# Performance work log

Measured on AMD Instinct MI355X. Metric: run time of the kernel, lower is better.

The kernel has to match this reference:

```python
import jax, jax.numpy as jnp
import numpy as np

EMB = 1024
HEADS = 16
HEAD_DIM = EMB // HEADS


def setup_inputs() -> dict:
    key = jax.random.key(0)
    ks = jax.random.split(key, 5)
    x = jax.random.normal(ks[0], (2, 2048, EMB), dtype=jnp.float32)
    # per-head projection params, stacked over heads: [H, E, D]
    Wq = jax.random.normal(ks[1], (HEADS, EMB, HEAD_DIM), dtype=jnp.float32)
    Wk = jax.random.normal(ks[2], (HEADS, EMB, HEAD_DIM), dtype=jnp.float32)
    Wv = jax.random.normal(ks[3], (HEADS, EMB, HEAD_DIM), dtype=jnp.float32)
    # output projection (torch Linear weight [out, in], bias=False)
    Wo = jax.random.normal(ks[4], (EMB, EMB), dtype=jnp.float32) * (1.0 / np.sqrt(EMB))
    return {"x": x, "Wq": Wq, "Wk": Wk, "Wv": Wv, "Wo": Wo}


def reference(x, Wq, Wk, Wv, Wo):
    B, T, E = x.shape
    # per-head projections: [B, H, T, D]
    q = jnp.einsum('bte,hed->bhtd', x, Wq)
    k = jnp.einsum('bte,hed->bhtd', x, Wk)
    v = jnp.einsum('bte,hed->bhtd', x, Wv)
    scale = 1.0 / jnp.sqrt(jnp.asarray(HEAD_DIM, dtype=x.dtype))
    scores = jnp.einsum('bhtd,bhsd->bhts', q, k) * scale  # [B,H,T,T]
    s = jax.nn.softmax(scores, axis=-1)
    out = jnp.einsum('bhts,bhsd->bhtd', s, v)
    # concat heads along last dim in head order: [B, T, H*D]
    combined = jnp.transpose(out, (0, 2, 1, 3)).reshape(B, T, E)
    # residual + output projection (Linear bias=False: y = combined @ Wo.T)
    return x + combined @ Wo.T
```

## Files before the change

kernel.cpp:

```cpp
#include <hip/hip_runtime.h>

#define EMB   1024
#define HEADS 16
#define HDIM  64
#define BATCH 2
#define SEQ   2048
#define MROWS (BATCH*SEQ)
#define STR   40
#define QSCALE 0.1803368801111204f

typedef __attribute__((ext_vector_type(8))) short bf16x8;
typedef __attribute__((ext_vector_type(4))) float f32x4;
typedef unsigned short u16;

__device__ __forceinline__ u16 f2bf(float f) {
    unsigned u = __float_as_uint(f);
    u += 0x7fffu + ((u >> 16) & 1u);
    return (u16)(u >> 16);
}
__device__ __forceinline__ float bf2f(u16 h) {
    return __uint_as_float((unsigned)h << 16);
}
__device__ __forceinline__ float fast_exp2(float x) {
#if __has_builtin(__builtin_amdgcn_exp2f)
    return __builtin_amdgcn_exp2f(x);
#else
    return __expf(x * 0.6931471805599453f);
#endif
}
__device__ __forceinline__ unsigned pk_trunc(float lo, float hi) {
    return __builtin_amdgcn_perm(__float_as_uint(hi), __float_as_uint(lo),
                                 0x07060302u);
}

#define SWZ(r, ch) ((((r) << 6)) + ((((ch) ^ ((r) & 7))) << 3))

__global__ __launch_bounds__(256)
void prep1(const float* __restrict__ X, const float* __restrict__ Wq,
           const float* __restrict__ Wk, const float* __restrict__ Wv,
           u16* __restrict__ Xh, u16* __restrict__ Xl,
           u16* __restrict__ Qth, u16* __restrict__ Qtl,
           u16* __restrict__ Kth, u16* __restrict__ Ktl,
           u16* __restrict__ Vth)
{
    const int bx = blockIdx.x;
    if (bx < 2048) {
        int i = (bx * 256 + threadIdx.x) * 8;
#pragma unroll
        for (int half = 0; half < 2; ++half) {
            float4 v = *(const float4*)(X + i + half * 4);
            ushort4 hi, lo;
            hi.x = f2bf(v.x); lo.x = f2bf(v.x - bf2f(hi.x));
            hi.y = f2bf(v.y); lo.y = f2bf(v.y - bf2f(hi.y));
            hi.z = f2bf(v.z); lo.z = f2bf(v.z - bf2f(hi.z));
            hi.w = f2bf(v.w); lo.w = f2bf(v.w - bf2f(hi.w));
            *(ushort4*)(Xh + i + half * 4) = hi;
            *(ushort4*)(Xl + i + half * 4) = lo;
        }
    } else if (bx < 3072) {
        const int f = bx - 2048;
        const int z = f >> 9, y = (f >> 5) & 15, x = f & 31;
        const float* W  = z ? Wk  : Wq;
        u16* Oh         = z ? Kth : Qth;
        u16* Ol         = z ? Ktl : Qtl;
        const int d  = threadIdx.x & 63;
        const int e0 = (x * 4 + (threadIdx.x >> 6)) * 8;
        const float* src = W + ((size_t)y * EMB + e0) * HDIM + d;
        ushort4 h0, h1, l0, l1;
        float v; u16 hv;
        v = src[0 * 64]; hv = f2bf(v); h0.x = hv; l0.x = f2bf(v - bf2f(hv));
        v = src[1 * 64]; hv = f2bf(v); h0.y = hv; l0.y = f2bf(v - bf2f(hv));
        v = src[2 * 64]; hv = f2bf(v); h0.z = hv; l0.z = f2bf(v - bf2f(hv));
        v = src[3 * 64]; hv = f2bf(v); h0.w = hv; l0.w = f2bf(v - bf2f(hv));
        v = src[4 * 64]; hv = f2bf(v); h1.x = hv; l1.x = f2bf(v - bf2f(hv));
        v = src[5 * 64]; hv = f2bf(v); h1.y = hv; l1.y = f2bf(v - bf2f(hv));
        v = src[6 * 64]; hv = f2bf(v); h1.z = hv; l1.z = f2bf(v - bf2f(hv));
        v = src[7 * 64]; hv = f2bf(v); h1.w = hv; l1.w = f2bf(v - bf2f(hv));
        size_t obase = ((size_t)y * HDIM + d) * EMB + e0;
        *(ushort4*)(Oh + obase)     = h0;
        *(ushort4*)(Oh + obase + 4) = h1;
        *(ushort4*)(Ol + obase)     = l0;
        *(ushort4*)(Ol + obase + 4) = l1;
    } else {
        const int f = bx - 3072;
        const int y = f >> 5, x = f & 31;
        const int d  = threadIdx.x & 63;
        const int e0 = (x * 4 + (threadIdx.x >> 6)) * 8;
        const float* src = Wv + ((size_t)y * EMB + e0) * HDIM + d;
        ushort4 h0, h1;
        h0.x = f2bf(src[0 * 64]); h0.y = f2bf(src[1 * 64]);
        h0.z = f2bf(src[2 * 64]); h0.w = f2bf(src[3 * 64]);
        h1.x = f2bf(src[4 * 64]); h1.y = f2bf(src[5 * 64]);
        h1.z = f2bf(src[6 * 64]); h1.w = f2bf(src[7 * 64]);
        size_t obase = ((size_t)y * HDIM + d) * EMB + e0;
        *(ushort4*)(Vth + obase)     = h0;
        *(ushort4*)(Vth + obase + 4) = h1;
    }
}

__global__ __launch_bounds__(256, 2)
void qkv_fused(const u16* __restrict__ Xh, const u16* __restrict__ Xl,
               const u16* __restrict__ Wqh, const u16* __restrict__ Wql,
               const u16* __restrict__ Wkh, const u16* __restrict__ Wkl,
               const u16* __restrict__ Wvt,
               u16* __restrict__ Qh, u16* __restrict__ Ql,
               u16* __restrict__ Kh, u16* __restrict__ Kl,
               u16* __restrict__ Vt)
{
    const int z  = blockIdx.z;
    const bool isV = (z == 2);
    const int m0 = blockIdx.x * 128;
    const int n0 = blockIdx.y * 128;
    const int t    = threadIdx.x;
    const int wave = t >> 6, lane = t & 63;
    const int wm = wave & 1, wn = wave >> 1;
    const int l16 = lane & 15, quad = lane >> 4;

    __shared__ u16 Ahs[128][STR];
    __shared__ u16 Als[128][STR];
    __shared__ u16 Bhs[128][STR];
    __shared__ u16 Bls[128][STR];

    const u16* Bh_g = isV ? Wvt : (z ? Wkh : Wqh);
    const u16* Bl_g = z ? Wkl : Wql;

    const int ar0 = t >> 2, ak = (t & 3) * 8, ar1 = ar0 + 64;

    f32x4 acc[4][4];
#pragma unroll
    for (int i = 0; i < 4; ++i)
#pragma unroll
        for (int j = 0; j < 4; ++j) acc[i][j] = (f32x4){0.f, 0.f, 0.f, 0.f};

    bf16x8 cur[8], nxt[8], nx2[8];
#define QK_LOAD(dst, kk)                                                            \
    do {                                                                            \
        dst[0] = *(const bf16x8*)(Xh  + (size_t)(m0 + ar0) * EMB + (kk) + ak);      \
        dst[1] = *(const bf16x8*)(Xh  + (size_t)(m0 + ar1) * EMB + (kk) + ak);      \
        dst[4] = *(const bf16x8*)(Bh_g + (size_t)(n0 + ar0) * EMB + (kk) + ak);     \
        dst[5] = *(const bf16x8*)(Bh_g + (size_t)(n0 + ar1) * EMB + (kk) + ak);     \
        if (!isV) {                                                                 \
            dst[2] = *(const bf16x8*)(Xl  + (size_t)(m0 + ar0) * EMB + (kk) + ak);  \
            dst[3] = *(const bf16x8*)(Xl  + (size_t)(m0 + ar1) * EMB + (kk) + ak);  \
            dst[6] = *(const bf16x8*)(Bl_g + (size_t)(n0 + ar0) * EMB + (kk) + ak); \
            dst[7] = *(const bf16x8*)(Bl_g + (size_t)(n0 + ar1) * EMB + (kk) + ak); \
        }                                                                           \
    } while (0)

    QK_LOAD(cur, 0);
    QK_LOAD(nxt, 32);

    for (int k0 = 0; k0 < EMB; k0 += 32) {
        __syncthreads();
        *(bf16x8*)&Ahs[ar0][ak] = cur[0];  *(bf16x8*)&Ahs[ar1][ak] = cur[1];
        *(bf16x8*)&Bhs[ar0][ak] = cur[4];  *(bf16x8*)&Bhs[ar1][ak] = cur[5];
        if (!isV) {
            *(bf16x8*)&Als[ar0][ak] = cur[2];  *(bf16x8*)&Als[ar1][ak] = cur[3];
            *(bf16x8*)&Bls[ar0][ak] = cur[6];  *(bf16x8*)&Bls[ar1][ak] = cur[7];
        }
        __syncthreads();

        const int kn = (k0 + 64 < EMB) ? k0 + 64 : 0;
        QK_LOAD(nx2, kn);

        bf16x8 B4h[4], B4l[4];
#pragma unroll
        for (int j = 0; j < 4; ++j) {
            B4h[j] = *(const bf16x8*)&Bhs[wn * 64 + 16 * j + l16][quad * 8];
            if (!isV)
                B4l[j] = *(const bf16x8*)&Bls[wn * 64 + 16 * j + l16][quad * 8];
        }
#pragma unroll
        for (int i = 0; i < 4; ++i) {
            bf16x8 Ai_h = *(const bf16x8*)&Ahs[wm * 64 + 16 * i + l16][quad * 8];
            if (!isV) {
                bf16x8 Ai_l = *(const bf16x8*)&Als[wm * 64 + 16 * i + l16][quad * 8];
#pragma unroll
                for (int j = 0; j < 4; ++j) {
                    acc[i][j] = __builtin_amdgcn_mfma_f32_16x16x32_bf16(Ai_h, B4h[j], acc[i][j], 0, 0, 0);
                    acc[i][j] = __builtin_amdgcn_mfma_f32_16x16x32_bf16(Ai_h, B4l[j], acc[i][j], 0, 0, 0);
                    acc[i][j] = __builtin_amdgcn_mfma_f32_16x16x32_bf16(Ai_l, B4h[j], acc[i][j], 0, 0, 0);
                }
            } else {
#pragma unroll
                for (int j = 0; j < 4; ++j)
                    acc[i][j] = __builtin_amdgcn_mfma_f32_16x16x32_bf16(Ai_h, B4h[j], acc[i][j], 0, 0, 0);
            }
        }
#pragma unroll
        for (int q = 0; q < 8; ++q) { cur[q] = nxt[q]; nxt[q] = nx2[q]; }
    }
#undef QK_LOAD

    const int b = m0 >> 11;
    const int h = (n0 + wn * 64) >> 6;
    if (isV) {
#pragma unroll
        for (int i = 0; i < 4; ++i)
#pragma unroll
            for (int j = 0; j < 4; ++j) {
                int d  = 16 * j + l16;
                int tt = (m0 & (SEQ - 1)) + wm * 64 + 16 * i + quad * 4;
                ushort4 o;
                o.x = f2bf(acc[i][j][0]); o.y = f2bf(acc[i][j][1]);
                o.z = f2bf(acc[i][j][2]); o.w = f2bf(acc[i][j][3]);
                *(ushort4*)(Vt + ((size_t)(b * HEADS + h) * HDIM + d) * SEQ + tt) = o;
            }
    } else {
        u16* Oh = z ? Kh : Qh;
        u16* Ol = z ? Kl : Ql;
        const float esc = z ? 1.0f : QSCALE;
#pragma unroll
        for (int i = 0; i < 4; ++i)
#pragma unroll
            for (int r = 0; r < 4; ++r) {
                int tt = (m0 & (SEQ - 1)) + wm * 64 + 16 * i + quad * 4 + r;
                size_t rowbase = ((size_t)(b * HEADS + h) * SEQ + tt) * HDIM;
#pragma unroll
                for (int j = 0; j < 4; ++j) {
                    int d = 16 * j + l16;
                    float v = acc[i][j][r] * esc;
                    u16 hv = f2bf(v);
                    Oh[rowbase + d] = hv;
                    Ol[rowbase + d] = f2bf(v - bf2f(hv));
                }
            }
    }
}

__global__ __launch_bounds__(256, 2)
void attn_mfma(const u16* __restrict__ Qh, const u16* __restrict__ Ql,
               const u16* __restrict__ Kh, const u16* __restrict__ Kl,
               const u16* __restrict__ Vt, u16* __restrict__ Cb,
               const float* __restrict__ Wo, u16* __restrict__ Woh)
{
    if (blockIdx.y == BATCH * HEADS) {
        int base = (blockIdx.x * 256 + threadIdx.x) * 8;
#pragma unroll 4
        for (int it = 0; it < 32; ++it) {
#pragma unroll
            for (int half = 0; half < 2; ++half) {
                float4 v = *(const float4*)(Wo + base + half * 4);
                ushort4 o;
                o.x = f2bf(v.x); o.y = f2bf(v.y); o.z = f2bf(v.z); o.w = f2bf(v.w);
                *(ushort4*)(Woh + base + half * 4) = o;
            }
            base += 16 * 256 * 8;
        }
        return;
    }

    const int qt0  = blockIdx.x * 128;
    const int bh   = blockIdx.y;
    const int t    = threadIdx.x;
    const int wave = t >> 6;
    const int lane = t & 63;
    const int l16  = lane & 15;
    const int quad = lane >> 4;

    __shared__ u16 Ksh[4096];
    __shared__ u16 Ksl[4096];
    __shared__ u16 Vs [4096];
    __shared__ u16 Ps [8192];

    const size_t bh_off = (size_t)bh * SEQ * HDIM;
    const u16* Qhb = Qh + bh_off;
    const u16* Qlb = Ql + bh_off;
    const u16* Khb = Kh + bh_off;
    const u16* Klb = Kl + bh_off;
    const u16* Vtb = Vt + bh_off;

    bf16x8 aQh[2][2], aQl[2][2];
#pragma unroll
    for (int g = 0; g < 2; ++g) {
        const int qrow = qt0 + g * 64 + wave * 16 + l16;
        const u16* bH = Qhb + (size_t)qrow * HDIM + quad * 8;
        const u16* bL = Qlb + (size_t)qrow * HDIM + quad * 8;
        aQh[g][0] = *(const bf16x8*)(bH);
        aQh[g][1] = *(const bf16x8*)(bH + 32);
        aQl[g][0] = *(const bf16x8*)(bL);
        aQl[g][1] = *(const bf16x8*)(bL + 32);
    }

    f32x4 accO[2][4];
    float m_i[2] = {-1e30f, -1e30f}, l_i[2] = {0.f, 0.f};
#pragma unroll
    for (int g = 0; g < 2; ++g)
#pragma unroll
        for (int j = 0; j < 4; ++j) accO[g][j] = (f32x4){0.f, 0.f, 0.f, 0.f};

    const int sr0 = t >> 3, sch = t & 7, sr1 = sr0 + 32;
    const int gc  = sch * 8;
    const int so0 = SWZ(sr0, sch), so1 = SWZ(sr1, sch);

    bf16x8 cur[6], nxt[6];
#define KV_LOAD(dst, ss)                                                       \
    do {                                                                       \
        dst[0] = *(const bf16x8*)(Khb + (size_t)((ss) + sr0) * HDIM + gc);     \
        dst[1] = *(const bf16x8*)(Khb + (size_t)((ss) + sr1) * HDIM + gc);     \
        dst[2] = *(const bf16x8*)(Klb + (size_t)((ss) + sr0) * HDIM + gc);     \
        dst[3] = *(const bf16x8*)(Klb + (size_t)((ss) + sr1) * HDIM + gc);     \
        dst[4] = *(const bf16x8*)(Vtb + (size_t)sr0 * SEQ + (ss) + gc);        \
        dst[5] = *(const bf16x8*)(Vtb + (size_t)sr1 * SEQ + (ss) + gc);        \
    } while (0)

    KV_LOAD(cur, 0);

    for (int s0 = 0; s0 < SEQ; s0 += 64) {
        __syncthreads();
        *(bf16x8*)&Ksh[so0] = cur[0];  *(bf16x8*)&Ksh[so1] = cur[1];
        *(bf16x8*)&Ksl[so0] = cur[2];  *(bf16x8*)&Ksl[so1] = cur[3];
        *(bf16x8*)&Vs [so0] = cur[4];  *(bf16x8*)&Vs [so1] = cur[5];
        __syncthreads();

        const int sn = (s0 + 64 < SEQ) ? s0 + 64 : 0;
        KV_LOAD(nxt, sn);

        f32x4 accS[2][4];
#pragma unroll
        for (int g = 0; g < 2; ++g)
#pragma unroll
            for (int i = 0; i < 4; ++i) accS[g][i] = (f32x4){0.f, 0.f, 0.f, 0.f};
#pragma unroll
        for (int c = 0; c < 2; ++c) {
#pragma unroll
            for (int i = 0; i < 4; ++i) {
                bf16x8 kh_ = *(const bf16x8*)&Ksh[SWZ(16 * i + l16, 4 * c + quad)];
                bf16x8 kl_ = *(const bf16x8*)&Ksl[SWZ(16 * i + l16, 4 * c + quad)];
                accS[0][i] = __builtin_amdgcn_mfma_f32_16x16x32_bf16(kh_, aQh[0][c], accS[0][i], 0, 0, 0);
                accS[0][i] = __builtin_amdgcn_mfma_f32_16x16x32_bf16(kl_, aQh[0][c], accS[0][i], 0, 0, 0);
                accS[0][i] = __builtin_amdgcn_mfma_f32_16x16x32_bf16(kh_, aQl[0][c], accS[0][i], 0, 0, 0);
                accS[1][i] = __builtin_amdgcn_mfma_f32_16x16x32_bf16(kh_, aQh[1][c], accS[1][i], 0, 0, 0);
                accS[1][i] = __builtin_amdgcn_mfma_f32_16x16x32_bf16(kl_, aQh[1][c], accS[1][i], 0, 0, 0);
                accS[1][i] = __builtin_amdgcn_mfma_f32_16x16x32_bf16(kh_, aQl[1][c], accS[1][i], 0, 0, 0);
            }
        }

#pragma unroll
        for (int g = 0; g < 2; ++g) {
            float vmax = fmaxf(fmaxf(accS[g][0][0], accS[g][0][1]),
                               fmaxf(accS[g][0][2], accS[g][0][3]));
#pragma unroll
            for (int i = 1; i < 4; ++i)
                vmax = fmaxf(vmax, fmaxf(fmaxf(accS[g][i][0], accS[g][i][1]),
                                         fmaxf(accS[g][i][2], accS[g][i][3])));
            vmax = fmaxf(vmax, __shfl_xor(vmax, 16, 64));
            vmax = fmaxf(vmax, __shfl_xor(vmax, 32, 64));
            float mn   = fmaxf(m_i[g], vmax);
            float alph = fast_exp2(m_i[g] - mn);
            m_i[g] = mn;
            float P[4][4], s = 0.f;
#pragma unroll
            for (int i = 0; i < 4; ++i)
#pragma unroll
                for (int r = 0; r < 4; ++r) {
                    P[i][r] = fast_exp2(accS[g][i][r] - mn);
                    s += P[i][r];
                }
            s += __shfl_xor(s, 16, 64);
            s += __shfl_xor(s, 32, 64);
            l_i[g] = l_i[g] * alph + s;
#pragma unroll
            for (int j = 0; j < 4; ++j) accO[g][j] *= alph;

            const int prow = g * 64 + wave * 16 + l16;
#pragma unroll
            for (int i = 0; i < 4; ++i) {
                uint2 pv;
                pv.x = pk_trunc(P[i][0], P[i][1]);
                pv.y = pk_trunc(P[i][2], P[i][3]);
                *(uint2*)&Ps[SWZ(prow, 2 * i + (quad >> 1)) + ((quad & 1) << 2)] = pv;
            }
        }

#pragma unroll
        for (int c = 0; c < 2; ++c) {
            bf16x8 bP0 = *(const bf16x8*)&Ps[SWZ(wave * 16 + l16,      4 * c + quad)];
            bf16x8 bP1 = *(const bf16x8*)&Ps[SWZ(64 + wave * 16 + l16, 4 * c + quad)];
#pragma unroll
            for (int j = 0; j < 4; ++j) {
                bf16x8 aV = *(const bf16x8*)&Vs[SWZ(16 * j + l16, 4 * c + quad)];
                accO[0][j] = __builtin_amdgcn_mfma_f32_16x16x32_bf16(aV, bP0, accO[0][j], 0, 0, 0);
                accO[1][j] = __builtin_amdgcn_mfma_f32_16x16x32_bf16(aV, bP1, accO[1][j], 0, 0, 0);
            }
        }
#pragma unroll
        for (int q = 0; q < 6; ++q) cur[q] = nxt[q];
    }
#undef KV_LOAD

    const int b = bh >> 4, h = bh & 15;
#pragma unroll
    for (int g = 0; g < 2; ++g) {
        const int row = qt0 + g * 64 + wave * 16 + l16;
        const float inv = 1.f / l_i[g];
#pragma unroll
        for (int j = 0; j < 4; ++j) {
            ushort4 o;
            o.x = f2bf(accO[g][j][0] * inv); o.y = f2bf(accO[g][j][1] * inv);
            o.z = f2bf(accO[g][j][2] * inv); o.w = f2bf(accO[g][j][3] * inv);
            *(ushort4*)&Cb[((size_t)b * SEQ + row) * EMB + h * HDIM + 16 * j + quad * 4] = o;
        }
    }
}

__global__ __launch_bounds__(256, 2)
void oproj_mfma(const u16* __restrict__ Cb, const u16* __restrict__ Woh,
                const float* __restrict__ X, float* __restrict__ Y)
{
    const int m0 = blockIdx.x * 128;
    const int n0 = blockIdx.y * 128;
    const int t    = threadIdx.x;
    const int wave = t >> 6, lane = t & 63;
    const int wm = wave & 1, wn = wave >> 1;
    const int l16 = lane & 15, quad = lane >> 4;

    __shared__ u16 Ahs[128][STR];
    __shared__ u16 Bhs[128][STR];

    const int ar0 = t >> 2, ak = (t & 3) * 8, ar1 = ar0 + 64;

    f32x4 acc[4][4];
#pragma unroll
    for (int i = 0; i < 4; ++i)
#pragma unroll
        for (int j = 0; j < 4; ++j) acc[i][j] = (f32x4){0.f, 0.f, 0.f, 0.f};

    bf16x8 cur[4], nxt[4], nx2[4];
#define O_LOAD(dst, kk)                                                         \
    do {                                                                        \
        dst[0] = *(const bf16x8*)(Cb  + (size_t)(m0 + ar0) * EMB + (kk) + ak);  \
        dst[1] = *(const bf16x8*)(Cb  + (size_t)(m0 + ar1) * EMB + (kk) + ak);  \
        dst[2] = *(const bf16x8*)(Woh + (size_t)(n0 + ar0) * EMB + (kk) + ak);  \
        dst[3] = *(const bf16x8*)(Woh + (size_t)(n0 + ar1) * EMB + (kk) + ak);  \
    } while (0)

    O_LOAD(cur, 0);
    O_LOAD(nxt, 32);

    for (int k0 = 0; k0 < EMB; k0 += 32) {
        __syncthreads();
        *(bf16x8*)&Ahs[ar0][ak] = cur[0];  *(bf16x8*)&Ahs[ar1][ak] = cur[1];
        *(bf16x8*)&Bhs[ar0][ak] = cur[2];  *(bf16x8*)&Bhs[ar1][ak] = cur[3];
        __syncthreads();

        const int kn = (k0 + 64 < EMB) ? k0 + 64 : 0;
        O_LOAD(nx2, kn);

        bf16x8 B4[4];
#pragma unroll
        for (int j = 0; j < 4; ++j)
            B4[j] = *(const bf16x8*)&Bhs[wn * 64 + 16 * j + l16][quad * 8];
#pragma unroll
        for (int i = 0; i < 4; ++i) {
            bf16x8 Ai = *(const bf16x8*)&Ahs[wm * 64 + 16 * i + l16][quad * 8];
#pragma unroll
            for (int j = 0; j < 4; ++j)
                acc[i][j] = __builtin_amdgcn_mfma_f32_16x16x32_bf16(Ai, B4[j], acc[i][j], 0, 0, 0);
        }
#pragma unroll
        for (int q = 0; q < 4; ++q) { cur[q] = nxt[q]; nxt[q] = nx2[q]; }
    }
#undef O_LOAD

#pragma unroll
    for (int i = 0; i < 4; ++i)
#pragma unroll
        for (int r = 0; r < 4; ++r) {
            int m = m0 + wm * 64 + 16 * i + quad * 4 + r;
#pragma unroll
            for (int j = 0; j < 4; ++j) {
                int n = n0 + wn * 64 + 16 * j + l16;
                Y[(size_t)m * EMB + n] = acc[i][j][r] + X[(size_t)m * EMB + n];
            }
        }
}

extern "C" void kernel_launch(void* const* d_in, const int* in_sizes, int n_in,
                              void* d_out, int out_size, void* d_ws,
                              size_t ws_size, hipStream_t stream)
{
    const float* x  = (const float*)d_in[0];
    const float* Wq = (const float*)d_in[1];
    const float* Wk = (const float*)d_in[2];
    const float* Wv = (const float*)d_in[3];
    const float* Wo = (const float*)d_in[4];
    float* Y = (float*)d_out;

    const size_t NPER = (size_t)MROWS * EMB;
    u16* base  = (u16*)d_ws;
    u16* Qh    = base;
    u16* Ql    = Qh + NPER;
    u16* Kh    = Ql + NPER;
    u16* Kl    = Kh + NPER;
    u16* Vt    = Kl + NPER;
    u16* Xh    = Vt + NPER;
    u16* Xl    = Xh + NPER;
    u16* Wtq_h = Xl + NPER;
    u16* Wtq_l = Wtq_h + EMB * EMB;
    u16* Wtk_h = Wtq_l + EMB * EMB;
    u16* Wtk_l = Wtk_h + EMB * EMB;
    u16* Wvt   = (u16*)d_out;
    u16* Cb    = Xh;
    u16* Woh   = Xl;

    prep1<<<dim3(3584), 256, 0, stream>>>(x, Wq, Wk, Wv, Xh, Xl,
                                          Wtq_h, Wtq_l, Wtk_h, Wtk_l, Wvt);
    qkv_fused<<<dim3(32, 8, 3), 256, 0, stream>>>(Xh, Xl, Wtq_h, Wtq_l,
                                                  Wtk_h, Wtk_l, Wvt,
                                                  Qh, Ql, Kh, Kl, Vt);
    attn_mfma<<<dim3(SEQ / 128, BATCH * HEADS + 1), 256, 0, stream>>>(
        Qh, Ql, Kh, Kl, Vt, Cb, Wo, Woh);
    oproj_mfma<<<dim3(32, 8), 256, 0, stream>>>(Cb, Woh, x, Y);
}
```

Baseline: 262.4 us.

## Halve attention query tile, remap blocks by head, and halve oproj M tile

```diff
diff --git a/kernel.cpp b/kernel.cpp
--- a/kernel.cpp
+++ b/kernel.cpp
@@ -228,14 +228,15 @@
     }
 }
 
-__global__ __launch_bounds__(256, 2)
+__global__ __launch_bounds__(256, 4)
 void attn_mfma(const u16* __restrict__ Qh, const u16* __restrict__ Ql,
                const u16* __restrict__ Kh, const u16* __restrict__ Kl,
                const u16* __restrict__ Vt, u16* __restrict__ Cb,
                const float* __restrict__ Wo, u16* __restrict__ Woh)
 {
-    if (blockIdx.y == BATCH * HEADS) {
-        int base = (blockIdx.x * 256 + threadIdx.x) * 8;
+    const int w = blockIdx.x;
+    if (w >= 1024) {
+        int base = ((w - 1024) * 256 + threadIdx.x) * 8;
 #pragma unroll 4
         for (int it = 0; it < 32; ++it) {
 #pragma unroll
@@ -250,8 +251,10 @@
         return;
     }
 
-    const int qt0  = blockIdx.x * 128;
-    const int bh   = blockIdx.y;
+    const int g    = w >> 3;
+    const int qt0  = (g & 31) * 64;
+    const int bh   = (w & 7) + ((g >> 5) << 3);
+
     const int t    = threadIdx.x;
     const int wave = t >> 6;
     const int lane = t & 63;
@@ -261,7 +264,7 @@
     __shared__ u16 Ksh[4096];
     __shared__ u16 Ksl[4096];
     __shared__ u16 Vs [4096];
-    __shared__ u16 Ps [8192];
+    __shared__ u16 Ps [4096];
 
     const size_t bh_off = (size_t)bh * SEQ * HDIM;
     const u16* Qhb = Qh + bh_off;
@@ -270,24 +273,21 @@
     const u16* Klb = Kl + bh_off;
     const u16* Vtb = Vt + bh_off;
 
-    bf16x8 aQh[2][2], aQl[2][2];
-#pragma unroll
-    for (int g = 0; g < 2; ++g) {
-        const int qrow = qt0 + g * 64 + wave * 16 + l16;
+    const int qrow = qt0 + wave * 16 + l16;
+    bf16x8 aQh[2], aQl[2];
+    {
         const u16* bH = Qhb + (size_t)qrow * HDIM + quad * 8;
         const u16* bL = Qlb + (size_t)qrow * HDIM + quad * 8;
-        aQh[g][0] = *(const bf16x8*)(bH);
-        aQh[g][1] = *(const bf16x8*)(bH + 32);
-        aQl[g][0] = *(const bf16x8*)(bL);
-        aQl[g][1] = *(const bf16x8*)(bL + 32);
-    }
-
-    f32x4 accO[2][4];
-    float m_i[2] = {-1e30f, -1e30f}, l_i[2] = {0.f, 0.f};
-#pragma unroll
-    for (int g = 0; g < 2; ++g)
-#pragma unroll
-        for (int j = 0; j < 4; ++j) accO[g][j] = (f32x4){0.f, 0.f, 0.f, 0.f};
+        aQh[0] = *(const bf16x8*)(bH);
+        aQh[1] = *(const bf16x8*)(bH + 32);
+        aQl[0] = *(const bf16x8*)(bL);
+        aQl[1] = *(const bf16x8*)(bL + 32);
+    }
+
+    f32x4 accO[4];
+    float m_i = -1e30f, l_i = 0.f;
+#pragma unroll
+    for (int j = 0; j < 4; ++j) accO[j] = (f32x4){0.f, 0.f, 0.f, 0.f};
 
     const int sr0 = t >> 3, sch = t & 7, sr1 = sr0 + 32;
     const int gc  = sch * 8;
@@ -316,54 +316,50 @@
         const int sn = (s0 + 64 < SEQ) ? s0 + 64 : 0;
         KV_LOAD(nxt, sn);
 
-        f32x4 accS[2][4];
-#pragma unroll
-        for (int g = 0; g < 2; ++g)
-#pragma unroll
-            for (int i = 0; i < 4; ++i) accS[g][i] = (f32x4){0.f, 0.f, 0.f, 0.f};
+        f32x4 accS[4];
+#pragma unroll
+        for (int i = 0; i < 4; ++i) accS[i] = (f32x4){0.f, 0.f, 0.f, 0.f};
+        __builtin_amdgcn_s_setprio(1);
 #pragma unroll
         for (int c = 0; c < 2; ++c) {
 #pragma unroll
             for (int i = 0; i < 4; ++i) {
                 bf16x8 kh_ = *(const bf16x8*)&Ksh[SWZ(16 * i + l16, 4 * c + quad)];
                 bf16x8 kl_ = *(const bf16x8*)&Ksl[SWZ(16 * i + l16, 4 * c + quad)];
-                accS[0][i] = __builtin_amdgcn_mfma_f32_16x16x32_bf16(kh_, aQh[0][c], accS[0][i], 0, 0, 0);
-                accS[0][i] = __builtin_amdgcn_mfma_f32_16x16x32_bf16(kl_, aQh[0][c], accS[0][i], 0, 0, 0);
-                accS[0][i] = __builtin_amdgcn_mfma_f32_16x16x32_bf16(kh_, aQl[0][c], accS[0][i], 0, 0, 0);
-                accS[1][i] = __builtin_amdgcn_mfma_f32_16x16x32_bf16(kh_, aQh[1][c], accS[1][i], 0, 0, 0);
-                accS[1][i] = __builtin_amdgcn_mfma_f32_16x16x32_bf16(kl_, aQh[1][c], accS[1][i], 0, 0, 0);
-                accS[1][i] = __builtin_amdgcn_mfma_f32_16x16x32_bf16(kh_, aQl[1][c], accS[1][i], 0, 0, 0);
-            }
-        }
-
-#pragma unroll
-        for (int g = 0; g < 2; ++g) {
-            float vmax = fmaxf(fmaxf(accS[g][0][0], accS[g][0][1]),
-                               fmaxf(accS[g][0][2], accS[g][0][3]));
+                accS[i] = __builtin_amdgcn_mfma_f32_16x16x32_bf16(kh_, aQh[c], accS[i], 0, 0, 0);
+                accS[i] = __builtin_amdgcn_mfma_f32_16x16x32_bf16(kl_, aQh[c], accS[i], 0, 0, 0);
+                accS[i] = __builtin_amdgcn_mfma_f32_16x16x32_bf16(kh_, aQl[c], accS[i], 0, 0, 0);
+            }
+        }
+        __builtin_amdgcn_s_setprio(0);
+
+        {
+            float vmax = fmaxf(fmaxf(accS[0][0], accS[0][1]),
+                               fmaxf(accS[0][2], accS[0][3]));
 #pragma unroll
             for (int i = 1; i < 4; ++i)
-                vmax = fmaxf(vmax, fmaxf(fmaxf(accS[g][i][0], accS[g][i][1]),
-                                         fmaxf(accS[g][i][2], accS[g][i][3])));
+                vmax = fmaxf(vmax, fmaxf(fmaxf(accS[i][0], accS[i][1]),
+                                         fmaxf(accS[i][2], accS[i][3])));
             vmax = fmaxf(vmax, __shfl_xor(vmax, 16, 64));
             vmax = fmaxf(vmax, __shfl_xor(vmax, 32, 64));
-            float mn   = fmaxf(m_i[g], vmax);
-            float alph = fast_exp2(m_i[g] - mn);
-            m_i[g] = mn;
+            float mn   = fmaxf(m_i, vmax);
+            float alph = fast_exp2(m_i - mn);
+            m_i = mn;
             float P[4][4], s = 0.f;
 #pragma unroll
             for (int i = 0; i < 4; ++i)
 #pragma unroll
                 for (int r = 0; r < 4; ++r) {
-                    P[i][r] = fast_exp2(accS[g][i][r] - mn);
+                    P[i][r] = fast_exp2(accS[i][r] - mn);
                     s += P[i][r];
                 }
             s += __shfl_xor(s, 16, 64);
             s += __shfl_xor(s, 32, 64);
-            l_i[g] = l_i[g] * alph + s;
-#pragma unroll
-            for (int j = 0; j < 4; ++j) accO[g][j] *= alph;
-
-            const int prow = g * 64 + wave * 16 + l16;
+            l_i = l_i * alph + s;
+#pragma unroll
+            for (int j = 0; j < 4; ++j) accO[j] *= alph;
+
+            const int prow = wave * 16 + l16;
 #pragma unroll
             for (int i = 0; i < 4; ++i) {
                 uint2 pv;
@@ -373,32 +369,31 @@
             }
         }
 
+        __builtin_amdgcn_s_setprio(1);
 #pragma unroll
         for (int c = 0; c < 2; ++c) {
-            bf16x8 bP0 = *(const bf16x8*)&Ps[SWZ(wave * 16 + l16,      4 * c + quad)];
-            bf16x8 bP1 = *(const bf16x8*)&Ps[SWZ(64 + wave * 16 + l16, 4 * c + quad)];
+            bf16x8 bP = *(const bf16x8*)&Ps[SWZ(wave * 16 + l16, 4 * c + quad)];
 #pragma unroll
             for (int j = 0; j < 4; ++j) {
                 bf16x8 aV = *(const bf16x8*)&Vs[SWZ(16 * j + l16, 4 * c + quad)];
-                accO[0][j] = __builtin_amdgcn_mfma_f32_16x16x32_bf16(aV, bP0, accO[0][j], 0, 0, 0);
-                accO[1][j] = __builtin_amdgcn_mfma_f32_16x16x32_bf16(aV, bP1, accO[1][j], 0, 0, 0);
-            }
-        }
+                accO[j] = __builtin_amdgcn_mfma_f32_16x16x32_bf16(aV, bP, accO[j], 0, 0, 0);
+            }
+        }
+        __builtin_amdgcn_s_setprio(0);
 #pragma unroll
         for (int q = 0; q < 6; ++q) cur[q] = nxt[q];
     }
 #undef KV_LOAD
 
     const int b = bh >> 4, h = bh & 15;
-#pragma unroll
-    for (int g = 0; g < 2; ++g) {
-        const int row = qt0 + g * 64 + wave * 16 + l16;
-        const float inv = 1.f / l_i[g];
+    {
+        const int row = qt0 + wave * 16 + l16;
+        const float inv = 1.f / l_i;
 #pragma unroll
         for (int j = 0; j < 4; ++j) {
             ushort4 o;
-            o.x = f2bf(accO[g][j][0] * inv); o.y = f2bf(accO[g][j][1] * inv);
-            o.z = f2bf(accO[g][j][2] * inv); o.w = f2bf(accO[g][j][3] * inv);
+            o.x = f2bf(accO[j][0] * inv); o.y = f2bf(accO[j][1] * inv);
+            o.z = f2bf(accO[j][2] * inv); o.w = f2bf(accO[j][3] * inv);
             *(ushort4*)&Cb[((size_t)b * SEQ + row) * EMB + h * HDIM + 16 * j + quad * 4] = o;
         }
     }
@@ -408,31 +403,30 @@
 void oproj_mfma(const u16* __restrict__ Cb, const u16* __restrict__ Woh,
                 const float* __restrict__ X, float* __restrict__ Y)
 {
-    const int m0 = blockIdx.x * 128;
+    const int m0 = blockIdx.x * 64;
     const int n0 = blockIdx.y * 128;
     const int t    = threadIdx.x;
     const int wave = t >> 6, lane = t & 63;
     const int wm = wave & 1, wn = wave >> 1;
     const int l16 = lane & 15, quad = lane >> 4;
 
-    __shared__ u16 Ahs[128][STR];
+    __shared__ u16 Ahs[64][STR];
     __shared__ u16 Bhs[128][STR];
 
     const int ar0 = t >> 2, ak = (t & 3) * 8, ar1 = ar0 + 64;
 
-    f32x4 acc[4][4];
-#pragma unroll
-    for (int i = 0; i < 4; ++i)
+    f32x4 acc[2][4];
+#pragma unroll
+    for (int i = 0; i < 2; ++i)
 #pragma unroll
         for (int j = 0; j < 4; ++j) acc[i][j] = (f32x4){0.f, 0.f, 0.f, 0.f};
 
-    bf16x8 cur[4], nxt[4], nx2[4];
+    bf16x8 cur[3], nxt[3], nx2[3];
 #define O_LOAD(dst, kk)                                                         \
     do {                                                                        \
         dst[0] = *(const bf16x8*)(Cb  + (size_t)(m0 + ar0) * EMB + (kk) + ak);  \
-        dst[1] = *(const bf16x8*)(Cb  + (size_t)(m0 + ar1) * EMB + (kk) + ak);  \
-        dst[2] = *(const bf16x8*)(Woh + (size_t)(n0 + ar0) * EMB + (kk) + ak);  \
-        dst[3] = *(const bf16x8*)(Woh + (size_t)(n0 + ar1) * EMB + (kk) + ak);  \
+        dst[1] = *(const bf16x8*)(Woh + (size_t)(n0 + ar0) * EMB + (kk) + ak);  \
+        dst[2] = *(const bf16x8*)(Woh + (size_t)(n0 + ar1) * EMB + (kk) + ak);  \
     } while (0)
 
     O_LOAD(cur, 0);
@@ -440,8 +434,8 @@
 
     for (int k0 = 0; k0 < EMB; k0 += 32) {
         __syncthreads();
-        *(bf16x8*)&Ahs[ar0][ak] = cur[0];  *(bf16x8*)&Ahs[ar1][ak] = cur[1];
-        *(bf16x8*)&Bhs[ar0][ak] = cur[2];  *(bf16x8*)&Bhs[ar1][ak] = cur[3];
+        *(bf16x8*)&Ahs[ar0][ak] = cur[0];
+        *(bf16x8*)&Bhs[ar0][ak] = cur[1];  *(bf16x8*)&Bhs[ar1][ak] = cur[2];
         __syncthreads();
 
         const int kn = (k0 + 64 < EMB) ? k0 + 64 : 0;
@@ -452,22 +446,22 @@
         for (int j = 0; j < 4; ++j)
             B4[j] = *(const bf16x8*)&Bhs[wn * 64 + 16 * j + l16][quad * 8];
 #pragma unroll
-        for (int i = 0; i < 4; ++i) {
-            bf16x8 Ai = *(const bf16x8*)&Ahs[wm * 64 + 16 * i + l16][quad * 8];
+        for (int i = 0; i < 2; ++i) {
+            bf16x8 Ai = *(const bf16x8*)&Ahs[wm * 32 + 16 * i + l16][quad * 8];
 #pragma unroll
             for (int j = 0; j < 4; ++j)
                 acc[i][j] = __builtin_amdgcn_mfma_f32_16x16x32_bf16(Ai, B4[j], acc[i][j], 0, 0, 0);
         }
 #pragma unroll
-        for (int q = 0; q < 4; ++q) { cur[q] = nxt[q]; nxt[q] = nx2[q]; }
+        for (int q = 0; q < 3; ++q) { cur[q] = nxt[q]; nxt[q] = nx2[q]; }
     }
 #undef O_LOAD
 
 #pragma unroll
-    for (int i = 0; i < 4; ++i)
+    for (int i = 0; i < 2; ++i)
 #pragma unroll
         for (int r = 0; r < 4; ++r) {
-            int m = m0 + wm * 64 + 16 * i + quad * 4 + r;
+            int m = m0 + wm * 32 + 16 * i + quad * 4 + r;
 #pragma unroll
             for (int j = 0; j < 4; ++j) {
                 int n = n0 + wn * 64 + 16 * j + l16;
@@ -509,7 +503,6 @@
     qkv_fused<<<dim3(32, 8, 3), 256, 0, stream>>>(Xh, Xl, Wtq_h, Wtq_l,
                                                   Wtk_h, Wtk_l, Wvt,
                                                   Qh, Ql, Kh, Kl, Vt);
-    attn_mfma<<<dim3(SEQ / 128, BATCH * HEADS + 1), 256, 0, stream>>>(
-        Qh, Ql, Kh, Kl, Vt, Cb, Wo, Woh);
-    oproj_mfma<<<dim3(32, 8), 256, 0, stream>>>(Cb, Woh, x, Y);
-}
+    attn_mfma<<<dim3(1040), 256, 0, stream>>>(Qh, Ql, Kh, Kl, Vt, Cb, Wo, Woh);
+    oproj_mfma<<<dim3(64, 8), 256, 0, stream>>>(Cb, Woh, x, Y);
+}
```

Measured after the change: 268.9 us. 1.02x slower.
